# Optimization experiments

Measured on AMD Instinct MI355X. Metric: run time of the kernel, lower is better.

## Reference

```python
import jax, jax.numpy as jnp
import numpy as np

R_MAX = 6.0
P = 6.0
QQ = 14.399645 * 0.5  # metal units, * 0.5


def setup_inputs() -> dict:
    key = jax.random.key(0)
    k1, k2, k3, k4 = jax.random.split(key, 4)
    n_atoms = 100_000
    n_edges = 6_400_000
    num_types = 4
    # atomic numbers for H, C, O, Cu
    Z = jnp.asarray([1.0, 6.0, 8.0, 29.0], dtype=jnp.float32)
    # edge lengths in (0.1, 7.3) so some edges exceed r_max and get cut off
    r = jax.random.uniform(k1, (n_edges,), dtype=jnp.float32) * 7.2 + 0.1
    per_atom_energy = jax.random.normal(k2, (n_atoms, 1), dtype=jnp.float32)
    atom_types = jax.random.randint(k3, (n_atoms,), 0, num_types, dtype=jnp.int64)
    edge_index = jax.random.randint(k4, (2, n_edges), 0, n_atoms, dtype=jnp.int64)
    return {"Z": Z, "r": r, "per_atom_energy": per_atom_energy,
            "atom_types": atom_types, "edge_index": edge_index}


def _zbl_edge_energy(Z, r, atom_types, edge_index):
    pzbl = 0.23
    a0 = 0.4685
    c1, c2, c3, c4 = 0.02817, 0.28022, 0.50986, 0.18175
    d1, d2, d3, d4 = -0.20162, -0.4029, -0.94229, -3.1998
    edge_types = atom_types[edge_index]          # (2, E)
    Zpair = Z[edge_types]                        # (2, E)
    Zi, Zj = Zpair[0], Zpair[1]
    x = (jnp.power(Zi, pzbl) + jnp.power(Zj, pzbl)) * r / a0
    psi = (c1 * jnp.exp(d1 * x) + c2 * jnp.exp(d2 * x)
           + c3 * jnp.exp(d3 * x) + c4 * jnp.exp(d4 * x))
    eng = QQ * (Zi * Zj / r) * psi
    rr = r / R_MAX
    p = P
    cutoff = (1.0 - (p + 1.0) * (p + 2.0) / 2.0 * jnp.power(rr, p)
              + p * (p + 2.0) * jnp.power(rr, p + 1.0)
              - p * (p + 1.0) / 2.0 * jnp.power(rr, p + 2.0))
    cutoff = cutoff * (rr < 1.0).astype(cutoff.dtype)
    return cutoff * eng                          # (E,)


def reference(Z, r, per_atom_energy, atom_types, edge_index):
    edge_eng = _zbl_edge_energy(Z, r, atom_types, edge_index)
    n_atoms = per_atom_energy.shape[0]
    atomic_eng = jax.ops.segment_sum(edge_eng, edge_index[0],
                                     num_segments=n_atoms)[:, None]
    return atomic_eng + per_atom_energy
```

## Files before the change

kernel.cpp:

```cpp
#include <hip/hip_runtime.h>


namespace {
constexpr float PZBL     = 0.23f;
constexpr float A0_INV   = 1.0f / 0.4685f;
constexpr float C1 = 0.02817f, C2 = 0.28022f, C3 = 0.50986f, C4 = 0.18175f;
constexpr float D1 = -0.20162f, D2 = -0.4029f, D3 = -0.94229f, D4 = -3.1998f;
constexpr float QQ       = 14.399645f * 0.5f;
constexpr float RMAX     = 6.0f;
constexpr float RMAX_INV = 1.0f / 6.0f;
constexpr int   TPW_MAX  = 6400;
constexpr int   P1_BLOCK = 256;
constexpr int   P1_GRID  = 1536;
constexpr int   CHUNK2   = 33344;
constexpr int   BLOCK    = 1024;
constexpr int   NXCD     = 8;
constexpr int   SPX      = 10;
constexpr int   CHUNK1   = 25600;
constexpr int   S1_MAX   = 64;
}

__global__ void zbl_pack_types(const int* __restrict__ types,
                               unsigned* __restrict__ tpw,
                               int n_words, int n_atoms) {
    int w = blockIdx.x * blockDim.x + threadIdx.x;
    if (w >= n_words) return;
    unsigned v = 0;
    int base = w * 16;
    int m = min(16, n_atoms - base);
    for (int j = 0; j < m; ++j)
        v |= ((unsigned)types[base + j] & 3u) << (2 * j);
    tpw[w] = v;
}

__device__ __forceinline__ float edge_eng_lds(float rk, int ia, int ib,
                                              const unsigned* s_tp,
                                              const float* s_zz,
                                              const float* s_zx) {
    unsigned ti = (s_tp[ia >> 4] >> ((ia & 15) * 2)) & 3u;
    unsigned tj = (s_tp[ib >> 4] >> ((ib & 15) * 2)) & 3u;
    int tp = (int)((ti << 2) | tj);
    float x = s_zx[tp] * rk;
    float psi = C1 * __expf(D1 * x) + C2 * __expf(D2 * x)
              + C3 * __expf(D3 * x) + C4 * __expf(D4 * x);
    float eng = s_zz[tp] * psi * __builtin_amdgcn_rcpf(rk);
    float rr = rk * RMAX_INV;
    float rr2 = rr * rr;
    float rr3 = rr2 * rr;
    float rr6 = rr3 * rr3;
    float cutoff = 1.0f + rr6 * (-28.0f + rr * (48.0f - 21.0f * rr));
    return (rk < RMAX) ? cutoff * eng : 0.0f;
}

__device__ __forceinline__ unsigned pack_rec(int dest, float e) {
    unsigned b = __float_as_uint(e);
    unsigned v = (b + 0x8000u) >> 16;
    return ((unsigned)dest << 15) | (v & 0x7FFFu);
}

__global__ __launch_bounds__(P1_BLOCK) void zbl_energy_kernel(
    const float*    __restrict__ Z,
    const float*    __restrict__ r,
    const int*      __restrict__ ei0,
    const int*      __restrict__ ei1,
    const unsigned* __restrict__ tpw,
    unsigned*       __restrict__ rec,
    int n_tp_words, int n_oct, int n_edges) {
    __shared__ unsigned s_tp[TPW_MAX];
    __shared__ float    s_zz[16];
    __shared__ float    s_zx[16];

    const int tid = threadIdx.x;
    for (int i = tid; i < n_tp_words; i += P1_BLOCK) s_tp[i] = tpw[i];
    if (tid < 16) {
        int ti = tid >> 2, tj = tid & 3;
        float zi = Z[ti], zj = Z[tj];
        s_zz[tid] = QQ * zi * zj;
        s_zx[tid] = (powf(zi, PZBL) + powf(zj, PZBL)) * A0_INV;
    }
    __syncthreads();

    const float4* r4 = (const float4*)r;
    const int4*   a4 = (const int4*)ei0;
    const int4*   b4 = (const int4*)ei1;
    uint4*        rc4 = (uint4*)rec;
    const int stride = gridDim.x * P1_BLOCK;
    const int gtid = blockIdx.x * P1_BLOCK + tid;

    for (int o = gtid; o < n_oct; o += stride) {
        int qa = 2 * o, qb = 2 * o + 1;
        float4 rva = r4[qa], rvb = r4[qb];
        int4   ava = a4[qa], avb = a4[qb];
        int4   bva = b4[qa], bvb = b4[qb];
        uint4 wa, wb;
        wa.x = pack_rec(ava.x, edge_eng_lds(rva.x, ava.x, bva.x, s_tp, s_zz, s_zx));
        wa.y = pack_rec(ava.y, edge_eng_lds(rva.y, ava.y, bva.y, s_tp, s_zz, s_zx));
        wa.z = pack_rec(ava.z, edge_eng_lds(rva.z, ava.z, bva.z, s_tp, s_zz, s_zx));
        wa.w = pack_rec(ava.w, edge_eng_lds(rva.w, ava.w, bva.w, s_tp, s_zz, s_zx));
        wb.x = pack_rec(avb.x, edge_eng_lds(rvb.x, avb.x, bvb.x, s_tp, s_zz, s_zx));
        wb.y = pack_rec(avb.y, edge_eng_lds(rvb.y, avb.y, bvb.y, s_tp, s_zz, s_zx));
        wb.z = pack_rec(avb.z, edge_eng_lds(rvb.z, avb.z, bvb.z, s_tp, s_zz, s_zx));
        wb.w = pack_rec(avb.w, edge_eng_lds(rvb.w, avb.w, bvb.w, s_tp, s_zz, s_zx));
        rc4[qa] = wa;
        rc4[qb] = wb;
    }
    for (int e = 8 * n_oct + gtid; e < n_edges; e += stride) {
        int ia = ei0[e];
        rec[e] = pack_rec(ia, edge_eng_lds(r[e], ia, ei1[e], s_tp, s_zz, s_zx));
    }
}

__global__ __launch_bounds__(BLOCK) void zbl_bin_kernel(
    const uint4* __restrict__ rec4,
    const unsigned* __restrict__ rec,
    float*       __restrict__ partials,
    int n_chunks, int u4_per_slice, int n_u4, int n_records, int xcd_mode) {
    __shared__ __align__(16) float bins[CHUNK2];
    {
        float4* b4 = (float4*)bins;
        const float4 z4 = make_float4(0.f, 0.f, 0.f, 0.f);
        for (int i = threadIdx.x; i < CHUNK2 / 4; i += BLOCK) b4[i] = z4;
    }
    __syncthreads();

    int c, s;
    if (xcd_mode) {
        int x = blockIdx.x & (NXCD - 1);
        int j = blockIdx.x >> 3;
        c = j % 3;
        s = x * SPX + j / 3;
    } else {
        c = blockIdx.x % n_chunks;
        s = blockIdx.x / n_chunks;
    }
    const unsigned base = (unsigned)c * CHUNK2;

    auto lane = [&](unsigned w) {
        unsigned d = (w >> 15) - base;
        unsigned v = w & 0x7FFFu;
        if (d < (unsigned)CHUNK2 && v != 0u)
            atomicAdd(&bins[d], __uint_as_float(v << 16));
    };

    const int q0 = s * u4_per_slice;
    const int q1 = min(n_u4, q0 + u4_per_slice);
    const uint4 dead = make_uint4(0, 0, 0, 0);

    for (int q = q0 + threadIdx.x; q < q1; q += 8 * BLOCK) {
        uint4 p0 = rec4[q];
        uint4 p1 = (q + 1 * BLOCK < q1) ? rec4[q + 1 * BLOCK] : dead;
        uint4 p2 = (q + 2 * BLOCK < q1) ? rec4[q + 2 * BLOCK] : dead;
        uint4 p3 = (q + 3 * BLOCK < q1) ? rec4[q + 3 * BLOCK] : dead;
        uint4 p4 = (q + 4 * BLOCK < q1) ? rec4[q + 4 * BLOCK] : dead;
        uint4 p5 = (q + 5 * BLOCK < q1) ? rec4[q + 5 * BLOCK] : dead;
        uint4 p6 = (q + 6 * BLOCK < q1) ? rec4[q + 6 * BLOCK] : dead;
        uint4 p7 = (q + 7 * BLOCK < q1) ? rec4[q + 7 * BLOCK] : dead;
        lane(p0.x); lane(p0.y); lane(p0.z); lane(p0.w);
        lane(p1.x); lane(p1.y); lane(p1.z); lane(p1.w);
        lane(p2.x); lane(p2.y); lane(p2.z); lane(p2.w);
        lane(p3.x); lane(p3.y); lane(p3.z); lane(p3.w);
        lane(p4.x); lane(p4.y); lane(p4.z); lane(p4.w);
        lane(p5.x); lane(p5.y); lane(p5.z); lane(p5.w);
        lane(p6.x); lane(p6.y); lane(p6.z); lane(p6.w);
        lane(p7.x); lane(p7.y); lane(p7.z); lane(p7.w);
    }
    if (s == 0) {
        for (int e = 4 * n_u4 + threadIdx.x; e < n_records; e += BLOCK)
            lane(rec[e]);
    }
    __syncthreads();

    const size_t out_blk = (size_t)s * n_chunks + c;
    float4* dst = (float4*)(partials + out_blk * CHUNK2);
    const float4* src = (const float4*)bins;
    for (int i = threadIdx.x; i < CHUNK2 / 4; i += BLOCK) dst[i] = src[i];
}

__global__ void zbl_reduce_out(const float* __restrict__ pae,
                               const float* __restrict__ partials,
                               float* __restrict__ out,
                               int n_atoms, int n_chunks, int n_slices,
                               int chunk) {
    int a = blockIdx.x * blockDim.x + threadIdx.x;
    if (a >= n_atoms) return;
    int c = a / chunk;
    int i = a - c * chunk;
    const float* p = partials + (size_t)c * chunk + i;
    const size_t stride = (size_t)n_chunks * chunk;
    float s0 = 0.0f, s1 = 0.0f, s2 = 0.0f, s3 = 0.0f;
    int s = 0;
    for (; s + 4 <= n_slices; s += 4) {
        s0 += p[(size_t)(s + 0) * stride];
        s1 += p[(size_t)(s + 1) * stride];
        s2 += p[(size_t)(s + 2) * stride];
        s3 += p[(size_t)(s + 3) * stride];
    }
    for (; s < n_slices; ++s) s0 += p[(size_t)s * stride];
    out[a] = pae[a] + ((s0 + s1) + (s2 + s3));
}

__global__ __launch_bounds__(BLOCK) void zbl_chunk_kernel(
    const float*    __restrict__ Z,
    const float*    __restrict__ r,
    const int*      __restrict__ ei0,
    const int*      __restrict__ ei1,
    const unsigned* __restrict__ tpw,
    float*          __restrict__ partials,
    int n_chunks, int n_tp_words, int quads_per_slice,
    int n_quads, int n_edges) {
    __shared__ float    bins[CHUNK1];
    __shared__ unsigned s_tp[TPW_MAX];
    __shared__ float    s_zz[16];
    __shared__ float    s_zx[16];
    const int tid = threadIdx.x;
    for (int i = tid; i < n_tp_words; i += BLOCK) s_tp[i] = tpw[i];
    if (tid < 16) {
        int ti = tid >> 2, tj = tid & 3;
        float zi = Z[ti], zj = Z[tj];
        s_zz[tid] = QQ * zi * zj;
        s_zx[tid] = (powf(zi, PZBL) + powf(zj, PZBL)) * A0_INV;
    }
    for (int i = tid; i < CHUNK1; i += BLOCK) bins[i] = 0.0f;
    __syncthreads();
    const int c = blockIdx.x % n_chunks;
    const int s = blockIdx.x / n_chunks;
    const int base = c * CHUNK1;
    const int q0 = s * quads_per_slice;
    const int q1 = min(n_quads, q0 + quads_per_slice);
    for (int q = q0 + tid; q < q1; q += BLOCK) {
        int4 av = ((const int4*)ei0)[q];
        unsigned d0 = (unsigned)(av.x - base);
        unsigned d1 = (unsigned)(av.y - base);
        unsigned d2 = (unsigned)(av.z - base);
        unsigned d3 = (unsigned)(av.w - base);
        bool m0 = d0 < (unsigned)CHUNK1, m1 = d1 < (unsigned)CHUNK1;
        bool m2 = d2 < (unsigned)CHUNK1, m3 = d3 < (unsigned)CHUNK1;
        if (!(m0 | m1 | m2 | m3)) continue;
        float4 rv = ((const float4*)r)[q];
        int4   bv = ((const int4*)ei1)[q];
        if (m0) { float e = edge_eng_lds(rv.x, av.x, bv.x, s_tp, s_zz, s_zx);
                  if (e != 0.0f) atomicAdd(&bins[d0], e); }
        if (m1) { float e = edge_eng_lds(rv.y, av.y, bv.y, s_tp, s_zz, s_zx);
                  if (e != 0.0f) atomicAdd(&bins[d1], e); }
        if (m2) { float e = edge_eng_lds(rv.z, av.z, bv.z, s_tp, s_zz, s_zx);
                  if (e != 0.0f) atomicAdd(&bins[d2], e); }
        if (m3) { float e = edge_eng_lds(rv.w, av.w, bv.w, s_tp, s_zz, s_zx);
                  if (e != 0.0f) atomicAdd(&bins[d3], e); }
    }
    if (s == 0) {
        for (int e = 4 * n_quads + tid; e < n_edges; e += BLOCK) {
            int ia = ei0[e];
            unsigned d = (unsigned)(ia - base);
            if (d < (unsigned)CHUNK1) {
                float e2 = edge_eng_lds(r[e], ia, ei1[e], s_tp, s_zz, s_zx);
                if (e2 != 0.0f) atomicAdd(&bins[d], e2);
            }
        }
    }
    __syncthreads();
    float* dst = partials + (size_t)blockIdx.x * CHUNK1;
    for (int i = tid; i < CHUNK1; i += BLOCK) dst[i] = bins[i];
}

__global__ void zbl_init_out(const float* __restrict__ pae,
                             float* __restrict__ out, int n) {
    int i = blockIdx.x * blockDim.x + threadIdx.x;
    if (i < n) out[i] = pae[i];
}

__global__ __launch_bounds__(256) void zbl_edge_fallback(
    const float* __restrict__ Z,
    const float* __restrict__ r,
    const int*   __restrict__ ei0,
    const int*   __restrict__ ei1,
    const int*   __restrict__ types,
    float*       __restrict__ out,
    int n_edges) {
    __shared__ float s_z[4];
    __shared__ float s_zp[4];
    if (threadIdx.x < 4) {
        float z = Z[threadIdx.x];
        s_z[threadIdx.x]  = z;
        s_zp[threadIdx.x] = powf(z, PZBL);
    }
    __syncthreads();
    int e = blockIdx.x * blockDim.x + threadIdx.x;
    if (e >= n_edges) return;
    float rk = r[e];
    if (rk >= RMAX) return;
    int ia = ei0[e], ib = ei1[e];
    int ti = types[ia], tj = types[ib];
    float x = (s_zp[ti] + s_zp[tj]) * rk * A0_INV;
    float psi = C1 * __expf(D1 * x) + C2 * __expf(D2 * x)
              + C3 * __expf(D3 * x) + C4 * __expf(D4 * x);
    float eng = QQ * s_z[ti] * s_z[tj] * psi / rk;
    float rr = rk * RMAX_INV;
    float rr2 = rr * rr, rr3 = rr2 * rr, rr6 = rr3 * rr3;
    float cutoff = 1.0f + rr6 * (-28.0f + rr * (48.0f - 21.0f * rr));
    unsafeAtomicAdd(&out[ia], cutoff * eng);
}

extern "C" void kernel_launch(void* const* d_in, const int* in_sizes, int n_in,
                              void* d_out, int out_size, void* d_ws, size_t ws_size,
                              hipStream_t stream) {
    const float* Z     = (const float*)d_in[0];
    const float* r     = (const float*)d_in[1];
    const float* pae   = (const float*)d_in[2];
    const int*   types = (const int*)d_in[3];
    const int*   ei    = (const int*)d_in[4];

    const int n_edges = in_sizes[1];
    const int n_atoms = in_sizes[2];

    float* out = (float*)d_out;

    const int n_tp_words = (n_atoms + 15) / 16;
    const int n_quads    = (n_edges & 3) ? 0 : (n_edges >> 2);

    const size_t tp_bytes  = ((size_t)n_tp_words * 4 + 15) & ~(size_t)15;
    const size_t rec_bytes = ((size_t)n_edges * 4 + 15) & ~(size_t)15;

    const int nc2 = (n_atoms + CHUNK2 - 1) / CHUNK2;

    const int  S2_XCD = NXCD * SPX;
    const bool ws_ok_xcd =
        tp_bytes + rec_bytes +
        (size_t)nc2 * S2_XCD * CHUNK2 * sizeof(float) <= ws_size;
    const bool xcd_mode = (nc2 == 3) && ws_ok_xcd;

    int S2;
    if (xcd_mode) {
        S2 = S2_XCD;
    } else {
        S2 = (nc2 > 0) ? (256 / nc2) : 1;
        while (S2 > 4 &&
               tp_bytes + rec_bytes +
               (size_t)nc2 * S2 * CHUNK2 * sizeof(float) > ws_size) {
            --S2;
        }
    }
    const bool two_phase =
        n_tp_words <= TPW_MAX && n_atoms <= (1 << 17) && S2 >= 4 &&
        n_quads > 0 &&
        tp_bytes + rec_bytes + (size_t)nc2 * S2 * CHUNK2 * sizeof(float)
            <= ws_size;

    const int nc1 = (n_atoms + CHUNK1 - 1) / CHUNK1;
    const bool one_phase =
        n_tp_words <= TPW_MAX &&
        tp_bytes + (size_t)nc1 * S1_MAX * CHUNK1 * sizeof(float) <= ws_size;

    if (two_phase) {
        unsigned* tpw = (unsigned*)d_ws;
        unsigned* rec = (unsigned*)((char*)d_ws + tp_bytes);
        float* partials = (float*)((char*)d_ws + tp_bytes + rec_bytes);

        zbl_pack_types<<<(n_tp_words + 255) / 256, 256, 0, stream>>>(
            types, tpw, n_tp_words, n_atoms);

        const int n_oct = n_quads >> 1;
        zbl_energy_kernel<<<P1_GRID, P1_BLOCK, 0, stream>>>(
            Z, r, ei, ei + n_edges, tpw, rec, n_tp_words, n_oct, n_edges);

        const int n_u4 = n_edges >> 2;
        const int u4_per_slice = (n_u4 + S2 - 1) / S2;
        zbl_bin_kernel<<<nc2 * S2, BLOCK, 0, stream>>>(
            (const uint4*)rec, rec, partials, nc2, u4_per_slice, n_u4,
            n_edges, xcd_mode ? 1 : 0);

        zbl_reduce_out<<<(n_atoms + 255) / 256, 256, 0, stream>>>(
            pae, partials, out, n_atoms, nc2, S2, CHUNK2);
    } else if (one_phase) {
        unsigned* tpw = (unsigned*)d_ws;
        float* partials = (float*)((char*)d_ws + tp_bytes);

        zbl_pack_types<<<(n_tp_words + 255) / 256, 256, 0, stream>>>(
            types, tpw, n_tp_words, n_atoms);

        const int quads_per_slice = (n_quads + S1_MAX - 1) / S1_MAX;
        zbl_chunk_kernel<<<nc1 * S1_MAX, BLOCK, 0, stream>>>(
            Z, r, ei, ei + n_edges, tpw, partials,
            nc1, n_tp_words, quads_per_slice, n_quads, n_edges);

        zbl_reduce_out<<<(n_atoms + 255) / 256, 256, 0, stream>>>(
            pae, partials, out, n_atoms, nc1, S1_MAX, CHUNK1);
    } else {
        zbl_init_out<<<(n_atoms + 255) / 256, 256, 0, stream>>>(pae, out, n_atoms);
        zbl_edge_fallback<<<(n_edges + 255) / 256, 256, 0, stream>>>(
            Z, r, ei, ei + n_edges, types, out, n_edges);
    }
}
```

Measured before the change: 166.8 us.

## Replace two-phase record scatter with fused atomic accumulation into replicated buffers

```diff
diff --git a/kernel.cpp b/kernel.cpp
--- a/kernel.cpp
+++ b/kernel.cpp
@@ -12,6 +12,7 @@
 constexpr int   TPW_MAX  = 6400;
 constexpr int   P1_BLOCK = 256;
 constexpr int   P1_GRID  = 1536;
+constexpr int   REP      = 16;
 constexpr int   CHUNK2   = 33344;
 constexpr int   BLOCK    = 1024;
 constexpr int   NXCD     = 8;
@@ -51,6 +52,88 @@
     float cutoff = 1.0f + rr6 * (-28.0f + rr * (48.0f - 21.0f * rr));
     return (rk < RMAX) ? cutoff * eng : 0.0f;
 }
+
+
+__global__ void zbl_zero4(float4* __restrict__ p, int n4) {
+    int i = blockIdx.x * blockDim.x + threadIdx.x;
+    if (i < n4) p[i] = make_float4(0.f, 0.f, 0.f, 0.f);
+}
+
+__global__ __launch_bounds__(P1_BLOCK) void zbl_fused_kernel(
+    const float*    __restrict__ Z,
+    const float*    __restrict__ r,
+    const int*      __restrict__ ei0,
+    const int*      __restrict__ ei1,
+    const unsigned* __restrict__ tpw,
+    float*          __restrict__ rep,
+    int n_tp_words, int n_oct, int n_edges, int n_atoms) {
+    __shared__ unsigned s_tp[TPW_MAX];
+    __shared__ float    s_zz[16];
+    __shared__ float    s_zx[16];
+
+    const int tid = threadIdx.x;
+    for (int i = tid; i < n_tp_words; i += P1_BLOCK) s_tp[i] = tpw[i];
+    if (tid < 16) {
+        int ti = tid >> 2, tj = tid & 3;
+        float zi = Z[ti], zj = Z[tj];
+        s_zz[tid] = QQ * zi * zj;
+        s_zx[tid] = (powf(zi, PZBL) + powf(zj, PZBL)) * A0_INV;
+    }
+    __syncthreads();
+
+    float* my = rep + (size_t)(blockIdx.x & (REP - 1)) * n_atoms;
+
+    const float4* r4 = (const float4*)r;
+    const int4*   a4 = (const int4*)ei0;
+    const int4*   b4 = (const int4*)ei1;
+    const int stride = gridDim.x * P1_BLOCK;
+    const int gtid = blockIdx.x * P1_BLOCK + tid;
+
+    for (int o = gtid; o < n_oct; o += stride) {
+        int qa = 2 * o, qb = 2 * o + 1;
+        float4 rva = r4[qa], rvb = r4[qb];
+        int4   ava = a4[qa], avb = a4[qb];
+        int4   bva = b4[qa], bvb = b4[qb];
+        float e0 = edge_eng_lds(rva.x, ava.x, bva.x, s_tp, s_zz, s_zx);
+        float e1 = edge_eng_lds(rva.y, ava.y, bva.y, s_tp, s_zz, s_zx);
+        float e2 = edge_eng_lds(rva.z, ava.z, bva.z, s_tp, s_zz, s_zx);
+        float e3 = edge_eng_lds(rva.w, ava.w, bva.w, s_tp, s_zz, s_zx);
+        float e4 = edge_eng_lds(rvb.x, avb.x, bvb.x, s_tp, s_zz, s_zx);
+        float e5 = edge_eng_lds(rvb.y, avb.y, bvb.y, s_tp, s_zz, s_zx);
+        float e6 = edge_eng_lds(rvb.z, avb.z, bvb.z, s_tp, s_zz, s_zx);
+        float e7 = edge_eng_lds(rvb.w, avb.w, bvb.w, s_tp, s_zz, s_zx);
+        if (e0 != 0.0f) unsafeAtomicAdd(&my[ava.x], e0);
+        if (e1 != 0.0f) unsafeAtomicAdd(&my[ava.y], e1);
+        if (e2 != 0.0f) unsafeAtomicAdd(&my[ava.z], e2);
+        if (e3 != 0.0f) unsafeAtomicAdd(&my[ava.w], e3);
+        if (e4 != 0.0f) unsafeAtomicAdd(&my[avb.x], e4);
+        if (e5 != 0.0f) unsafeAtomicAdd(&my[avb.y], e5);
+        if (e6 != 0.0f) unsafeAtomicAdd(&my[avb.z], e6);
+        if (e7 != 0.0f) unsafeAtomicAdd(&my[avb.w], e7);
+    }
+    for (int e = 8 * n_oct + gtid; e < n_edges; e += stride) {
+        int ia = ei0[e];
+        float ee = edge_eng_lds(r[e], ia, ei1[e], s_tp, s_zz, s_zx);
+        if (ee != 0.0f) unsafeAtomicAdd(&my[ia], ee);
+    }
+}
+
+__global__ void zbl_reduce_rep(const float* __restrict__ pae,
+                               const float* __restrict__ rep,
+                               float* __restrict__ out, int n_atoms) {
+    int a = blockIdx.x * blockDim.x + threadIdx.x;
+    if (a >= n_atoms) return;
+    float s0 = 0.f, s1 = 0.f, s2 = 0.f, s3 = 0.f;
+    #pragma unroll
+    for (int k = 0; k < REP; k += 4) {
+        s0 += rep[(size_t)(k + 0) * n_atoms + a];
+        s1 += rep[(size_t)(k + 1) * n_atoms + a];
+        s2 += rep[(size_t)(k + 2) * n_atoms + a];
+        s3 += rep[(size_t)(k + 3) * n_atoms + a];
+    }
+    out[a] = pae[a] + ((s0 + s1) + (s2 + s3));
+}
+
 
 __device__ __forceinline__ unsigned pack_rec(int dest, float e) {
     unsigned b = __float_as_uint(e);
@@ -320,8 +403,33 @@
     const size_t tp_bytes  = ((size_t)n_tp_words * 4 + 15) & ~(size_t)15;
     const size_t rec_bytes = ((size_t)n_edges * 4 + 15) & ~(size_t)15;
 
+    const size_t rep_floats = ((size_t)REP * n_atoms + 3) & ~(size_t)3;
+    const size_t rep_bytes  = rep_floats * sizeof(float);
+    const bool fused_ok =
+        n_tp_words <= TPW_MAX && n_quads > 0 &&
+        tp_bytes + rep_bytes <= ws_size;
+
+    if (fused_ok) {
+        unsigned* tpw = (unsigned*)d_ws;
+        float*    rep = (float*)((char*)d_ws + tp_bytes);
+
+        zbl_pack_types<<<(n_tp_words + 255) / 256, 256, 0, stream>>>(
+            types, tpw, n_tp_words, n_atoms);
+
+        const int n4 = (int)(rep_floats / 4);
+        zbl_zero4<<<(n4 + 255) / 256, 256, 0, stream>>>((float4*)rep, n4);
+
+        const int n_oct = n_quads >> 1;
+        zbl_fused_kernel<<<P1_GRID, P1_BLOCK, 0, stream>>>(
+            Z, r, ei, ei + n_edges, tpw, rep, n_tp_words, n_oct,
+            n_edges, n_atoms);
+
+        zbl_reduce_rep<<<(n_atoms + 255) / 256, 256, 0, stream>>>(
+            pae, rep, out, n_atoms);
+        return;
+    }
+
     const int nc2 = (n_atoms + CHUNK2 - 1) / CHUNK2;
-
     const int  S2_XCD = NXCD * SPX;
     const bool ws_ok_xcd =
         tp_bytes + rec_bytes +
```

After: 358.2 us. +114.7%, slower.
